# Optimization experiments

Hardware: AMD Instinct MI355X
Metric: run time of the kernel (lower is better)

## Reference

```python
import jax, jax.numpy as jnp
import numpy as np

N, E = 100000, 800000
DIN, DH, DOUT = 128, 64, 16


def _glorot_linear(k, din, dout):
    s = 1.0 / np.sqrt(din)
    return jax.random.uniform(k, (din, dout), jnp.float32, -s, s)


def setup_inputs() -> dict:
    key = jax.random.key(0)
    ks = jax.random.split(key, 6)
    x = jax.random.normal(ks[0], (N, DIN), jnp.float32)
    edge_index = jax.random.randint(ks[1], (2, E), 0, N, dtype=jnp.int64)
    edge_attr = jax.random.uniform(ks[2], (E,), jnp.float32)  # positive edge weights
    W1 = _glorot_linear(ks[3], DIN, DH)
    b1 = jnp.zeros((DH,), jnp.float32)
    W2 = _glorot_linear(ks[4], DH, DH)
    b2 = jnp.zeros((DH,), jnp.float32)
    W3 = _glorot_linear(ks[5], DH, DOUT)
    b3 = jnp.zeros((DOUT,), jnp.float32)
    return {"x": x, "edge_index": edge_index, "edge_attr": edge_attr,
            "W1": W1, "b1": b1, "W2": W2, "b2": b2, "W3": W3, "b3": b3}


def gcn_conv(x, W, b, src, dst, ew, n):
    """PyG GCNConv: linear transform, add self-loops (weight 1), symmetric
    degree normalization, scatter-add aggregation (source_to_target), bias."""
    h = x @ W                                   # [N, dout]
    deg = jax.ops.segment_sum(ew, dst, num_segments=n) + 1.0  # +1 for self-loop
    dinv = jax.lax.rsqrt(deg)                   # deg >= 1 always
    norm = dinv[src] * ew * dinv[dst]           # [E]
    agg = jax.ops.segment_sum(h[src] * norm[:, None], dst, num_segments=n)
    # self-loop contribution: h[i] * dinv[i]^2
    return agg + h * (dinv * dinv)[:, None] + b


def reference(x, edge_index, edge_attr, W1, b1, W2, b2, W3, b3):
    src, dst = edge_index[0], edge_index[1]
    n = x.shape[0]
    h = jax.nn.relu(gcn_conv(x, W1, b1, src, dst, edge_attr, n))
    # dropout is identity in eval mode
    h = jax.nn.relu(gcn_conv(h, W2, b2, src, dst, edge_attr, n))
    h = gcn_conv(h, W3, b3, src, dst, edge_attr, n)
    return jax.nn.log_softmax(h, axis=1)
```

## Files before the change

### kernel.cpp

```cpp
#include <hip/hip_runtime.h>
#include <hip/hip_bf16.h>
#include <math.h>

#define DIN 128
#define DH 64
#define DOUT_ 16
#define SL 32
#define BSH 9
#define NBMAX 256
#define CAP 5120
#define CH 2048

typedef long long ll;
typedef __attribute__((ext_vector_type(8))) short bf16x8;
typedef __attribute__((ext_vector_type(4))) float f32x4;

__device__ inline ushort f2bf(float f) {
    unsigned u = __float_as_uint(f);
    u += 0x7FFF + ((u >> 16) & 1);
    return (ushort)(u >> 16);
}
__device__ inline float bf2f(ushort s) { return __uint_as_float(((unsigned)s) << 16); }

template <int K, int NC>
__device__ inline void stage_W(const float* __restrict__ W, ushort* __restrict__ Wt) {
    for (int t = threadIdx.x; t < (K / 8) * NC; t += 256) {
        int kblk = t / NC, c = t % NC;
        bf16x8 v;
        #pragma unroll
        for (int klo = 0; klo < 8; klo++)
            v[klo] = (short)f2bf(W[(kblk * 8 + klo) * NC + c]);
        *(bf16x8*)&Wt[t * 8] = v;
    }
}

__global__ __launch_bounds__(256) void bin_and_gemm(const int* __restrict__ src,
                                                    const int* __restrict__ dst,
                                                    const float* __restrict__ ew,
                                                    int* __restrict__ gcur,
                                                    int2* __restrict__ bins, int E,
                                                    const float* __restrict__ X,
                                                    const float* __restrict__ W,
                                                    ushort* __restrict__ H, int N,
                                                    int FB) {
    __shared__ int hist[NBMAX];
    __shared__ int curb[NBMAX];
    __shared__ int baseb[NBMAX];
    __shared__ __align__(16) ushort Wt[DIN * DH];

    const int tid = threadIdx.x;

    if (blockIdx.x < FB) {
        hist[tid] = 0;
        curb[tid] = 0;
        __syncthreads();
        const int e0 = blockIdx.x * CH;
        if (e0 + CH <= E) {
            const int r0 = e0 + tid * 4;
            const int r1 = r0 + 1024;
            int4 dA = *(const int4*)(dst + r0);
            int4 dB = *(const int4*)(dst + r1);
            int4 sA = *(const int4*)(src + r0);
            int4 sB = *(const int4*)(src + r1);
            float4 wA = *(const float4*)(ew + r0);
            float4 wB = *(const float4*)(ew + r1);
            atomicAdd(&hist[dA.x >> BSH], 1);
            atomicAdd(&hist[dA.y >> BSH], 1);
            atomicAdd(&hist[dA.z >> BSH], 1);
            atomicAdd(&hist[dA.w >> BSH], 1);
            atomicAdd(&hist[dB.x >> BSH], 1);
            atomicAdd(&hist[dB.y >> BSH], 1);
            atomicAdd(&hist[dB.z >> BSH], 1);
            atomicAdd(&hist[dB.w >> BSH], 1);
            __syncthreads();
            { int hc = hist[tid]; baseb[tid] = hc ? atomicAdd(&gcur[tid], hc) : 0; }
            __syncthreads();
            #define EMIT(dv, sv, wv)                                                    \
                {                                                                       \
                    int b_ = (dv) >> BSH;                                               \
                    int pos_ = baseb[b_] + atomicAdd(&curb[b_], 1);                     \
                    if (pos_ < CAP)                                                     \
                        bins[(ll)b_ * CAP + pos_] = make_int2(                          \
                            (sv) | (((dv) & ((1 << BSH) - 1)) << 20), __float_as_int(wv)); \
                }
            EMIT(dA.x, sA.x, wA.x)
            EMIT(dA.y, sA.y, wA.y)
            EMIT(dA.z, sA.z, wA.z)
            EMIT(dA.w, sA.w, wA.w)
            EMIT(dB.x, sB.x, wB.x)
            EMIT(dB.y, sB.y, wB.y)
            EMIT(dB.z, sB.z, wB.z)
            EMIT(dB.w, sB.w, wB.w)
            #undef EMIT
        } else {
            const int ecnt = E - e0;
            for (int r = tid; r < ecnt; r += 256)
                atomicAdd(&hist[dst[e0 + r] >> BSH], 1);
            __syncthreads();
            { int hc = hist[tid]; baseb[tid] = hc ? atomicAdd(&gcur[tid], hc) : 0; }
            __syncthreads();
            for (int r = tid; r < ecnt; r += 256) {
                int e = e0 + r;
                int d = dst[e];
                int b = d >> BSH;
                int pos = baseb[b] + atomicAdd(&curb[b], 1);
                if (pos < CAP)
                    bins[(ll)b * CAP + pos] =
                        make_int2(src[e] | ((d & ((1 << BSH) - 1)) << 20), __float_as_int(ew[e]));
            }
        }
        return;
    }

    const int bid = blockIdx.x - FB;
    stage_W<DIN, DH>(W, Wt);
    __syncthreads();

    const int wave = tid >> 6;
    const int lane = tid & 63;
    const int rowTile = bid * 64 + wave * 16;
    const int arow = rowTile + (lane & 15);
    const int kgrp = lane >> 4;

    f32x4 acc[DH / 16];
    #pragma unroll
    for (int cf = 0; cf < DH / 16; cf++) acc[cf] = (f32x4){0.f, 0.f, 0.f, 0.f};

    #pragma unroll
    for (int ks = 0; ks < DIN / 32; ks++) {
        const int k0 = ks * 32 + kgrp * 8;
        bf16x8 a = {0, 0, 0, 0, 0, 0, 0, 0};
        if (arow < N) {
            const float* xp = X + (ll)arow * DIN + k0;
            float4 f0 = ((const float4*)xp)[0];
            float4 f1 = ((const float4*)xp)[1];
            a[0] = (short)f2bf(f0.x); a[1] = (short)f2bf(f0.y);
            a[2] = (short)f2bf(f0.z); a[3] = (short)f2bf(f0.w);
            a[4] = (short)f2bf(f1.x); a[5] = (short)f2bf(f1.y);
            a[6] = (short)f2bf(f1.z); a[7] = (short)f2bf(f1.w);
        }
        #pragma unroll
        for (int cf = 0; cf < DH / 16; cf++) {
            bf16x8 b = *(const bf16x8*)&Wt[(((k0 >> 3) * DH) + cf * 16 + (lane & 15)) * 8];
            acc[cf] = __builtin_amdgcn_mfma_f32_16x16x32_bf16(a, b, acc[cf], 0, 0, 0);
        }
    }

    const int rbase = rowTile + kgrp * 4;
    #pragma unroll
    for (int cf = 0; cf < DH / 16; cf++) {
        #pragma unroll
        for (int r = 0; r < 4; r++) {
            int row = rbase + r;
            if (row < N)
                H[(ll)row * DH + cf * 16 + (lane & 15)] = f2bf(acc[cf][r]);
        }
    }
}

__global__ __launch_bounds__(512) void debin(const int2* __restrict__ bins,
                                             const int* __restrict__ gcur,
                                             int2* __restrict__ pair, int* __restrict__ cnt,
                                             float* __restrict__ dinv, int N) {
    __shared__ int cl[1 << BSH];
    __shared__ float wsum[1 << BSH];
    const int tid = threadIdx.x;
    for (int i = tid; i < (1 << BSH); i += 512) { cl[i] = 0; wsum[i] = 0.f; }
    __syncthreads();

    const int b = blockIdx.x;
    const int nbase = b << BSH;
    const int m = min(gcur[b], CAP);
    const int mv = m & ~1;
    const int2* bp = bins + (ll)b * CAP;
    for (int i = tid * 2; i < mv; i += 1024) {
        int4 t2 = *(const int4*)(bp + i);
        int dlo0 = t2.x >> 20, s0 = t2.x & 0xFFFFF;
        int dlo1 = t2.z >> 20, s1 = t2.z & 0xFFFFF;
        int slot0 = atomicAdd(&cl[dlo0], 1);
        int slot1 = atomicAdd(&cl[dlo1], 1);
        if (slot0 < SL) pair[(ll)(nbase + dlo0) * SL + slot0] = make_int2(s0, t2.y);
        if (slot1 < SL) pair[(ll)(nbase + dlo1) * SL + slot1] = make_int2(s1, t2.w);
        atomicAdd(&wsum[dlo0], __int_as_float(t2.y));
        atomicAdd(&wsum[dlo1], __int_as_float(t2.w));
    }
    if ((m & 1) && tid == 0) {
        int2 t = bp[m - 1];
        int dlo = t.x >> 20, s = t.x & 0xFFFFF;
        int slot = atomicAdd(&cl[dlo], 1);
        if (slot < SL) pair[(ll)(nbase + dlo) * SL + slot] = make_int2(s, t.y);
        atomicAdd(&wsum[dlo], __int_as_float(t.y));
    }
    __syncthreads();
    for (int i = tid; i < (1 << BSH); i += 512) {
        int node = nbase + i;
        if (node < N) {
            cnt[node] = min(cl[i], SL);
            dinv[node] = rsqrtf(wsum[i] + 1.0f);
        }
    }
}

template <int NC, bool SRC_DINV>
__global__ __launch_bounds__(256) void fused_gg(const ushort* __restrict__ h,
                                                const int2* __restrict__ pair,
                                                const int* __restrict__ cnt,
                                                const float* __restrict__ dinv,
                                                const float* __restrict__ bias,
                                                const float* __restrict__ W,
                                                ushort* __restrict__ Hout, int N) {
    __shared__ __align__(16) ushort Wt[64 * NC];
    __shared__ __align__(16) ushort Hs[64][72];

    stage_W<64, NC>(W, Wt);

    const int tid = threadIdx.x;
    const int grp = tid >> 3;
    const int l8 = tid & 7;
    const ushort* __restrict__ hb = h + l8 * 8;

    #pragma unroll
    for (int pass = 0; pass < 2; pass++) {
        int nl = pass * 32 + grp;
        int node = blockIdx.x * 64 + nl;
        float acc[8];
        #pragma unroll
        for (int j = 0; j < 8; j++) acc[j] = 0.f;
        bf16x8 outv = {0, 0, 0, 0, 0, 0, 0, 0};
        if (node < N) {
            int deg = min(cnt[node], SL);
            const int2* p = pair + (ll)node * SL;
            for (int e = 0; e < deg; e += 4) {
                int2 p0 = p[e];
                int2 p1 = p[e + 1];
                int2 p2 = p[e + 2];
                int2 p3 = p[e + 3];
                bool m1 = (e + 1 < deg), m2 = (e + 2 < deg), m3 = (e + 3 < deg);
                int s1 = m1 ? p1.x : 0;
                int s2 = m2 ? p2.x : 0;
                int s3 = m3 ? p3.x : 0;
                float w0 = __int_as_float(p0.y);
                float w1 = m1 ? __int_as_float(p1.y) : 0.f;
                float w2 = m2 ? __int_as_float(p2.y) : 0.f;
                float w3 = m3 ? __int_as_float(p3.y) : 0.f;
                if (SRC_DINV) {
                    w0 *= dinv[p0.x]; w1 *= dinv[s1];
                    w2 *= dinv[s2];   w3 *= dinv[s3];
                }
                bf16x8 a0 = *(const bf16x8*)(hb + (ll)p0.x * 64);
                bf16x8 a1 = *(const bf16x8*)(hb + (ll)s1 * 64);
                bf16x8 a2 = *(const bf16x8*)(hb + (ll)s2 * 64);
                bf16x8 a3 = *(const bf16x8*)(hb + (ll)s3 * 64);
                #pragma unroll
                for (int j = 0; j < 8; j++)
                    acc[j] += bf2f((ushort)a0[j]) * w0 + bf2f((ushort)a1[j]) * w1 +
                              bf2f((ushort)a2[j]) * w2 + bf2f((ushort)a3[j]) * w3;
            }
            float di = dinv[node];
            float sf = SRC_DINV ? di : 1.0f;
            bf16x8 hs = *(const bf16x8*)(hb + (ll)node * 64);
            float4 bv0 = ((const float4*)bias)[l8 * 2];
            float4 bv1 = ((const float4*)bias)[l8 * 2 + 1];
            float bv[8] = {bv0.x, bv0.y, bv0.z, bv0.w, bv1.x, bv1.y, bv1.z, bv1.w};
            #pragma unroll
            for (int j = 0; j < 8; j++) {
                float r = fmaxf(di * (acc[j] + bf2f((ushort)hs[j]) * sf) + bv[j], 0.f);
                outv[j] = (short)f2bf(r);
            }
        }
        *(bf16x8*)&Hs[nl][l8 * 8] = outv;
    }
    __syncthreads();

    const int wave = tid >> 6;
    const int lane = tid & 63;
    const int kgrp = lane >> 4;
    f32x4 acc2[NC / 16];
    #pragma unroll
    for (int cf = 0; cf < NC / 16; cf++) acc2[cf] = (f32x4){0.f, 0.f, 0.f, 0.f};

    #pragma unroll
    for (int ks = 0; ks < 2; ks++) {
        const int k0 = ks * 32 + kgrp * 8;
        bf16x8 a = *(const bf16x8*)&Hs[wave * 16 + (lane & 15)][k0];
        #pragma unroll
        for (int cf = 0; cf < NC / 16; cf++) {
            bf16x8 b = *(const bf16x8*)&Wt[(((k0 >> 3) * NC) + cf * 16 + (lane & 15)) * 8];
            acc2[cf] = __builtin_amdgcn_mfma_f32_16x16x32_bf16(a, b, acc2[cf], 0, 0, 0);
        }
    }

    const int rbase = blockIdx.x * 64 + wave * 16 + kgrp * 4;
    float dsc[4];
    #pragma unroll
    for (int r = 0; r < 4; r++) dsc[r] = (rbase + r < N) ? dinv[rbase + r] : 1.0f;
    #pragma unroll
    for (int cf = 0; cf < NC / 16; cf++) {
        #pragma unroll
        for (int r = 0; r < 4; r++) {
            int row = rbase + r;
            if (row < N)
                Hout[(ll)row * NC + cf * 16 + (lane & 15)] = f2bf(acc2[cf][r] * dsc[r]);
        }
    }
}

__global__ __launch_bounds__(256) void gather16_final(const ushort* __restrict__ h3,
                                                      const int2* __restrict__ pair,
                                                      const int* __restrict__ cnt,
                                                      const float* __restrict__ dinv,
                                                      const float* __restrict__ b3,
                                                      float* __restrict__ out, int N) {
    int node = blockIdx.x * 128 + (threadIdx.x >> 1);
    int l2 = threadIdx.x & 1;
    if (node >= N) return;
    int deg = min(cnt[node], SL);
    const int2* p = pair + (ll)node * SL;
    const ushort* __restrict__ hb = h3 + l2 * 8;

    float acc[8];
    #pragma unroll
    for (int j = 0; j < 8; j++) acc[j] = 0.f;
    for (int e = 0; e < deg; e += 4) {
        int2 p0 = p[e];
        int2 p1 = p[e + 1];
        int2 p2 = p[e + 2];
        int2 p3 = p[e + 3];
        bool m1 = (e + 1 < deg), m2 = (e + 2 < deg), m3 = (e + 3 < deg);
        int s1 = m1 ? p1.x : 0;
        int s2 = m2 ? p2.x : 0;
        int s3 = m3 ? p3.x : 0;
        float w0 = __int_as_float(p0.y);
        float w1 = m1 ? __int_as_float(p1.y) : 0.f;
        float w2 = m2 ? __int_as_float(p2.y) : 0.f;
        float w3 = m3 ? __int_as_float(p3.y) : 0.f;
        bf16x8 a0 = *(const bf16x8*)(hb + (ll)p0.x * 16);
        bf16x8 a1 = *(const bf16x8*)(hb + (ll)s1 * 16);
        bf16x8 a2 = *(const bf16x8*)(hb + (ll)s2 * 16);
        bf16x8 a3 = *(const bf16x8*)(hb + (ll)s3 * 16);
        #pragma unroll
        for (int j = 0; j < 8; j++)
            acc[j] += bf2f((ushort)a0[j]) * w0 + bf2f((ushort)a1[j]) * w1 +
                      bf2f((ushort)a2[j]) * w2 + bf2f((ushort)a3[j]) * w3;
    }

    float di = dinv[node];
    bf16x8 hs = *(const bf16x8*)(hb + (ll)node * 16);
    float4 bv0 = ((const float4*)b3)[l2 * 2];
    float4 bv1 = ((const float4*)b3)[l2 * 2 + 1];
    float bv[8] = {bv0.x, bv0.y, bv0.z, bv0.w, bv1.x, bv1.y, bv1.z, bv1.w};
    float z[8];
    #pragma unroll
    for (int j = 0; j < 8; j++)
        z[j] = di * (acc[j] + bf2f((ushort)hs[j])) + bv[j];

    float m = z[0];
    #pragma unroll
    for (int j = 1; j < 8; j++) m = fmaxf(m, z[j]);
    m = fmaxf(m, __shfl_xor(m, 1, 2));
    float s = 0.f;
    #pragma unroll
    for (int j = 0; j < 8; j++) s += expf(z[j] - m);
    s += __shfl_xor(s, 1, 2);
    float l = logf(s);

    float4 r0, r1;
    r0.x = z[0] - m - l; r0.y = z[1] - m - l; r0.z = z[2] - m - l; r0.w = z[3] - m - l;
    r1.x = z[4] - m - l; r1.y = z[5] - m - l; r1.z = z[6] - m - l; r1.w = z[7] - m - l;
    float4* o4 = (float4*)out + (ll)node * 4 + l2 * 2;
    o4[0] = r0;
    o4[1] = r1;
}

extern "C" void kernel_launch(void* const* d_in, const int* in_sizes, int n_in,
                              void* d_out, int out_size, void* d_ws, size_t ws_size,
                              hipStream_t stream) {
    const float* x = (const float*)d_in[0];
    const int* ei = (const int*)d_in[1];
    const float* ew = (const float*)d_in[2];
    const float* W1 = (const float*)d_in[3];
    const float* b1 = (const float*)d_in[4];
    const float* W2 = (const float*)d_in[5];
    const float* b2 = (const float*)d_in[6];
    const float* W3 = (const float*)d_in[7];
    const float* b3 = (const float*)d_in[8];

    const int N = in_sizes[0] / DIN;
    const int E = in_sizes[2];
    const int* src = ei;
    const int* dst = ei + E;

    float* out = (float*)d_out;

    int2* pair = (int2*)d_ws;
    ushort* A = (ushort*)(pair + (ll)N * SL);
    ushort* A2 = A + (ll)N * DH;
    ushort* C = A2 + (ll)N * DH;
    float* dinv = (float*)(C + (ll)N * DOUT_);
    int* cnt = (int*)(dinv + N);
    int* gcur = cnt + N;
    int2* bins = (int2*)A2;

    const int TB = 256;
    const int NB = (N + (1 << BSH) - 1) >> BSH;
    const int FB = (E + CH - 1) / CH;
    const int rowBlocks = (N + 63) / 64;

    hipMemsetAsync(gcur, 0, NBMAX * sizeof(int), stream);
    bin_and_gemm<<<FB + rowBlocks, TB, 0, stream>>>(src, dst, ew, gcur, bins, E,
                                                    x, W1, A, N, FB);
    debin<<<NB, 512, 0, stream>>>(bins, gcur, pair, cnt, dinv, N);

    fused_gg<DH, true><<<rowBlocks, TB, 0, stream>>>(A, pair, cnt, dinv, b1, W2, A2, N);

    fused_gg<DOUT_, false><<<rowBlocks, TB, 0, stream>>>(A2, pair, cnt, dinv, b2, W3, C, N);

    gather16_final<<<(N + 127) / 128, TB, 0, stream>>>(C, pair, cnt, dinv, b3, out, N);
}
```

Before: 110.7 us.

## Stage binned edges in shared memory to coalesce global bin writes

Edge records in the binning phase are first sorted by bin into an LDS staging buffer (reusing the Wt array), using a block-wide prefix scan over the bin histogram. They are then written out with consecutive threads covering consecutive sorted slots, and each thread finds its bin by binary search. The goal is to replace scattered 8-byte global stores with mostly contiguous runs per bin. The cost is the extra scan, several more syncthreads, and LDS traffic.

```diff
diff --git a/kernel.cpp b/kernel.cpp
--- a/kernel.cpp
+++ b/kernel.cpp
@@ -46,11 +46,13 @@
     __shared__ int hist[NBMAX];
     __shared__ int curb[NBMAX];
     __shared__ int baseb[NBMAX];
+    __shared__ int lbase[NBMAX + 1];
     __shared__ __align__(16) ushort Wt[DIN * DH];
 
     const int tid = threadIdx.x;
 
     if (blockIdx.x < FB) {
+        int2* stage = (int2*)Wt;
         hist[tid] = 0;
         curb[tid] = 0;
         __syncthreads();
@@ -73,25 +75,52 @@
             atomicAdd(&hist[dB.z >> BSH], 1);
             atomicAdd(&hist[dB.w >> BSH], 1);
             __syncthreads();
+            lbase[tid] = hist[tid];
+            __syncthreads();
+            for (int d = 1; d < NBMAX; d <<= 1) {
+                int t = (tid >= d) ? lbase[tid - d] : 0;
+                __syncthreads();
+                lbase[tid] += t;
+                __syncthreads();
+            }
+            int incl = lbase[tid];
+            int excl = incl - hist[tid];
             { int hc = hist[tid]; baseb[tid] = hc ? atomicAdd(&gcur[tid], hc) : 0; }
             __syncthreads();
-            #define EMIT(dv, sv, wv)                                                    \
+            lbase[tid] = excl;
+            if (tid == NBMAX - 1) lbase[NBMAX] = incl;
+            __syncthreads();
+            #define EMITS(dv, sv, wv)                                                   \
                 {                                                                       \
                     int b_ = (dv) >> BSH;                                               \
-                    int pos_ = baseb[b_] + atomicAdd(&curb[b_], 1);                     \
-                    if (pos_ < CAP)                                                     \
-                        bins[(ll)b_ * CAP + pos_] = make_int2(                          \
-                            (sv) | (((dv) & ((1 << BSH) - 1)) << 20), __float_as_int(wv)); \
+                    int off_ = atomicAdd(&curb[b_], 1);                                 \
+                    stage[lbase[b_] + off_] = make_int2(                                \
+                        (sv) | (((dv) & ((1 << BSH) - 1)) << 20), __float_as_int(wv));  \
                 }
-            EMIT(dA.x, sA.x, wA.x)
-            EMIT(dA.y, sA.y, wA.y)
-            EMIT(dA.z, sA.z, wA.z)
-            EMIT(dA.w, sA.w, wA.w)
-            EMIT(dB.x, sB.x, wB.x)
-            EMIT(dB.y, sB.y, wB.y)
-            EMIT(dB.z, sB.z, wB.z)
-            EMIT(dB.w, sB.w, wB.w)
-            #undef EMIT
+            EMITS(dA.x, sA.x, wA.x)
+            EMITS(dA.y, sA.y, wA.y)
+            EMITS(dA.z, sA.z, wA.z)
+            EMITS(dA.w, sA.w, wA.w)
+            EMITS(dB.x, sB.x, wB.x)
+            EMITS(dB.y, sB.y, wB.y)
+            EMITS(dB.z, sB.z, wB.z)
+            EMITS(dB.w, sB.w, wB.w)
+            #undef EMITS
+            __syncthreads();
+            #pragma unroll
+            for (int k = 0; k < CH / 256; k++) {
+                int i = k * 256 + tid;
+                int2 rec = stage[i];
+                int lo = 0, hi = NBMAX - 1;
+                #pragma unroll
+                for (int it = 0; it < 8; it++) {
+                    int mid = (lo + hi + 1) >> 1;
+                    if (lbase[mid] <= i) lo = mid; else hi = mid - 1;
+                }
+                int b = lo;
+                int pos = baseb[b] + (i - lbase[b]);
+                if (pos < CAP) bins[(ll)b * CAP + pos] = rec;
+            }
         } else {
             const int ecnt = E - e0;
             for (int r = tid; r < ecnt; r += 256)
```

After: 107.8 us. 1.03x faster.
